# Kernel optimization log

Measured on AMD Instinct MI355X. Metric: run time of the kernel, lower is better.

## Reference

```python
import jax, jax.numpy as jnp
import numpy as np

N, E, B, BLOCK = 100000, 1600000, 8, 12500
IN, HID, K, OUT = 128, 128, 4, 2
EPS = 1e-15


def setup_inputs() -> dict:
    key = jax.random.key(0)
    ks = jax.random.split(key, 14)
    x = jax.random.normal(ks[0], (N, IN), jnp.float32)
    # edges constrained within each graph's contiguous node block
    src = jax.random.randint(ks[1], (E,), 0, N)
    off = jax.random.randint(ks[2], (E,), 0, BLOCK)
    dst = (src // BLOCK) * BLOCK + off
    edge_index = jnp.stack([src, dst])
    batch = jnp.arange(N) // BLOCK
    s = 0.02
    params = dict(
        W_root1=jax.random.normal(ks[3], (IN, HID), jnp.float32) * s,
        W_rel1=jax.random.normal(ks[4], (IN, HID), jnp.float32) * s,
        b_rel1=jnp.zeros((HID,), jnp.float32),
        W_pool=jax.random.normal(ks[5], (HID, K), jnp.float32) * s,
        b_pool=jnp.zeros((K,), jnp.float32),
        W_rel3=jax.random.normal(ks[6], (HID, HID), jnp.float32) * s,
        b_rel3=jnp.zeros((HID,), jnp.float32),
        W_root3=jax.random.normal(ks[7], (HID, HID), jnp.float32) * s,
        W_lin1=jax.random.normal(ks[8], (HID, HID), jnp.float32) * s,
        b_lin1=jnp.zeros((HID,), jnp.float32),
        W_lin2=jax.random.normal(ks[9], (HID, OUT), jnp.float32) * s,
        b_lin2=jnp.zeros((OUT,), jnp.float32),
    )
    return dict(x=x, edge_index=edge_index, batch=batch, **params)


def _forward(x, edge_index, batch, W_root1, W_rel1, b_rel1, W_pool, b_pool,
             W_rel3, b_rel3, W_root3, W_lin1, b_lin1, W_lin2, b_lin2):
    src, dst = edge_index[0], edge_index[1]
    # GraphConv (aggr='add'): lin_rel(sum_j x_j) + lin_root(x)
    agg = jax.ops.segment_sum(x[src], dst, num_segments=N)  # [N, IN]
    h = jax.nn.relu(agg @ W_rel1 + b_rel1 + x @ W_root1)    # [N, HID]
    # cluster assignment
    s = jax.nn.softmax(h @ W_pool + b_pool, axis=-1)        # [N, K]
    # pooled node features: out[b] = S_b^T X_b  -> [B, K, HID]
    out = jax.ops.segment_sum(s[:, :, None] * h[:, None, :], batch, num_segments=B)
    # coarsened adjacency: out_adj[b] = S_b^T A_b S_b (A[dst, src] = 1 per edge)
    e_graph = batch[dst]
    contrib = s[dst][:, :, None] * s[src][:, None, :]       # [E, K, K]
    out_adj = jax.ops.segment_sum(contrib, e_graph, num_segments=B)  # [B, K, K]
    # mincut loss
    mincut_num = jnp.einsum('bkk->b', out_adj)
    deg = jax.ops.segment_sum(jnp.ones((E,), x.dtype), dst, num_segments=N)
    mincut_den = jax.ops.segment_sum(deg * jnp.sum(s * s, axis=-1), batch, num_segments=B)
    mc_loss = jnp.mean(-(mincut_num / mincut_den))
    # orthogonality loss
    ss = jax.ops.segment_sum(s[:, :, None] * s[:, None, :], batch, num_segments=B)  # [B,K,K]
    ss_norm = jnp.linalg.norm(ss, axis=(1, 2), keepdims=True)
    i_s = jnp.eye(K, dtype=x.dtype)
    o_loss = jnp.mean(jnp.linalg.norm(ss / ss_norm - i_s / jnp.sqrt(jnp.float32(K)), axis=(1, 2)))
    # fix and normalize coarsened adjacency
    out_adj = out_adj * (1.0 - i_s)  # zero diagonal
    d = jnp.sqrt(jnp.sum(out_adj, axis=-1)) + EPS  # [B, K]
    out_adj = out_adj / d[:, None, :] / d[:, :, None]
    # DenseGraphConv (aggr='add'): lin_rel(adj @ x) + lin_root(x)
    x2 = jnp.einsum('bkl,blc->bkc', out_adj, out) @ W_rel3 + b_rel3 + out @ W_root3
    x2 = jnp.mean(x2, axis=1)  # [B, HID]
    x2 = jax.nn.relu(x2 @ W_lin1 + b_lin1)
    logits = x2 @ W_lin2 + b_lin2
    return jax.nn.log_softmax(logits, axis=-1), mc_loss, o_loss, s, out_adj


def reference(x, edge_index, batch, W_root1, W_rel1, b_rel1, W_pool, b_pool,
              W_rel3, b_rel3, W_root3, W_lin1, b_lin1, W_lin2, b_lin2):
    return _forward(x, edge_index, batch, W_root1, W_rel1, b_rel1, W_pool, b_pool,
                    W_rel3, b_rel3, W_root3, W_lin1, b_lin1, W_lin2, b_lin2)
```

## Files before the change

kernel.cpp:

```cpp
#include <hip/hip_runtime.h>

#define NN     100000
#define EE     1600000
#define NB     8
#define BLK    12500
#define HID    128
#define KC     4
#define CHUNKS 196
#define NTILE  49
#define NBIN   392
#define GCAPS  5120

typedef __attribute__((ext_vector_type(8))) short bf16x8;
typedef __attribute__((ext_vector_type(4))) float f32x4;

__device__ __forceinline__ ushort f2bf(float f) {
  uint u = __float_as_uint(f);
  return (ushort)((u + 0x7FFFu + ((u >> 16) & 1u)) >> 16);
}
__device__ __forceinline__ float bf2f(ushort h) {
  return __uint_as_float(((uint)h) << 16);
}

__global__ __launch_bounds__(256) void k_prep_x(const float4* __restrict__ x4,
                                                ushort* __restrict__ xb) {
  int i = blockIdx.x * 256 + threadIdx.x;
  float4 v = x4[i];
  ushort4 r;
  r.x = f2bf(v.x); r.y = f2bf(v.y); r.z = f2bf(v.z); r.w = f2bf(v.w);
  *(ushort4*)(xb + (size_t)i * 4) = r;
}

__global__ __launch_bounds__(256) void k_prep_w(const float* __restrict__ Wrel1,
                                                const float* __restrict__ Wroot1,
                                                ushort* __restrict__ Wt) {
  int col = blockIdx.x, k = threadIdx.x;
  float v = (k < 128) ? Wrel1[k * 128 + col] : Wroot1[(k - 128) * 128 + col];
  Wt[col * 256 + k] = f2bf(v);
}

__global__ __launch_bounds__(256) void k_bucket2(const int* __restrict__ ei,
                                                 int* __restrict__ sbcnt,
                                                 uint* __restrict__ gbuf) {
  __shared__ uint stage[8192];
  __shared__ int cnt[NBIN], start[NBIN + 1], rbase[NBIN];
  __shared__ int gtot[8], gb[8];
  const int t = threadIdx.x;
  for (int b = t; b < NBIN; b += 256) cnt[b] = 0;
  __syncthreads();
  const int e0 = blockIdx.x * 8192;
  uint pk[32]; int br[32];
#pragma unroll
  for (int i = 0; i < 32; ++i) {
    int e = e0 + i * 256 + t;
    bool val = (e < EE);
    int src = 0, dst = 0;
    if (val) {
      src = __builtin_nontemporal_load(ei + e);
      dst = __builtin_nontemporal_load(ei + EE + e);
    }
    int g = dst / BLK;
    int dl = dst - g * BLK;
    int sl = src - g * BLK;
    int bin = g * NTILE + (dl >> 8);
    pk[i] = ((uint)sl << 16) | (uint)dl;
    br[i] = val ? ((bin << 14) | atomicAdd(&cnt[bin], 1)) : -1;
  }
  __syncthreads();
  if (t < 8) {
    int s = 0;
    for (int k = 0; k < NTILE; ++k) s += cnt[t * NTILE + k];
    gtot[t] = s;
  }
  __syncthreads();
  if (t == 0) {
    int s = 0;
    for (int g = 0; g < 8; ++g) { gb[g] = s; s += gtot[g]; }
    start[NBIN] = s;
  }
  __syncthreads();
  if (t < 8) {
    int run = gb[t];
    for (int k = 0; k < NTILE; ++k) { start[t * NTILE + k] = run; run += cnt[t * NTILE + k]; }
  }
  __syncthreads();
  for (int b = t; b < NBIN; b += 256) rbase[b] = atomicAdd(&sbcnt[b], cnt[b]);
#pragma unroll
  for (int i = 0; i < 32; ++i) {
    if (br[i] >= 0) {
      int bin = br[i] >> 14, rank = br[i] & 16383;
      stage[start[bin] + rank] = pk[i];
    }
  }
  __syncthreads();
  const int total = start[NBIN];
  for (int j = t; j < total; j += 256) {
    int lo = 0, hi = NBIN - 1;
    while (lo < hi) { int mid = (lo + hi + 1) >> 1; if (j >= start[mid]) lo = mid; else hi = mid - 1; }
    gbuf[(size_t)lo * GCAPS + rbase[lo] + (j - start[lo])] = stage[j];
  }
}

__global__ __launch_bounds__(512) void k_scan392(const int* __restrict__ sbcnt,
                                                 int* __restrict__ sbbase) {
  __shared__ int sd[512];
  const int t = threadIdx.x;
  int v = (t < NBIN) ? sbcnt[t] : 0;
  sd[t] = v;
  __syncthreads();
  for (int s = 1; s < 512; s <<= 1) {
    int x = (t >= s) ? sd[t - s] : 0;
    __syncthreads();
    sd[t] += x;
    __syncthreads();
  }
  if (t < NBIN) sbbase[t] = sd[t] - v;
}

__global__ __launch_bounds__(256) void k_csr_tile(const uint* __restrict__ gbuf,
                                                  const int* __restrict__ sbcnt,
                                                  const int* __restrict__ sbbase,
                                                  int* __restrict__ rowptr,
                                                  int* __restrict__ count,
                                                  int* __restrict__ csr) {
  const int g = blockIdx.x & 7;
  const int tile = blockIdx.x >> 3;
  const int bin = g * NTILE + tile;
  const int m = sbcnt[bin];
  const int base = sbbase[bin];
  const int n0t = tile * 256;
  const int nt = min(256, BLK - n0t);
  __shared__ uint ent[GCAPS];
  __shared__ ushort srt[GCAPS];
  __shared__ int cnt[256], scn[256], cur[256];
  const int t = threadIdx.x;
  cnt[t] = 0;
  __syncthreads();
  const uint* buf = gbuf + (size_t)bin * GCAPS;
  for (int i = t; i < m; i += 256) {
    uint pk = buf[i];
    ent[i] = pk;
    atomicAdd(&cnt[(int)(pk & 0xFFFFu) - n0t], 1);
  }
  __syncthreads();
  int v = cnt[t];
  scn[t] = v;
  __syncthreads();
  for (int s = 1; s < 256; s <<= 1) {
    int x = (t >= s) ? scn[t - s] : 0;
    __syncthreads();
    scn[t] += x;
    __syncthreads();
  }
  int excl = scn[t] - v;
  cur[t] = excl;
  if (t < nt) {
    rowptr[g * BLK + n0t + t] = base + excl;
    count[g * BLK + n0t + t] = v;
  }
  __syncthreads();
  for (int i = t; i < m; i += 256) {
    uint pk = ent[i];
    int p = atomicAdd(&cur[(int)(pk & 0xFFFFu) - n0t], 1);
    srt[p] = (ushort)(pk >> 16);
  }
  __syncthreads();
  const int nb = g * BLK;
  for (int i = t; i < m; i += 256)
    csr[base + i] = nb + (int)srt[i];
}

__global__ __launch_bounds__(256) void k_agg2(const ushort* __restrict__ xb,
                                              const int* __restrict__ count,
                                              const int* __restrict__ rowptr,
                                              const int* __restrict__ csr,
                                              ushort* __restrict__ aggb) {
  const int xg = blockIdx.x & 7;
  const int j = blockIdx.x >> 3;
  const int half = threadIdx.x >> 5;
  const int lane = threadIdx.x & 31;
  const int ln = j * 8 + half;
  if (ln >= BLK) return;
  const int node = xg * BLK + ln;
  const int deg = count[node];
  const int* sl = csr + rowptr[node];
  int idx0 = (lane < deg) ? sl[lane] : 0;
  int idx1 = (32 + lane < deg) ? sl[32 + lane] : 0;

#define GETIDX(e) ((e) < 32 ? __shfl(idx0, (e), 32) \
                            : ((e) < 64 ? __shfl(idx1, (e) - 32, 32) : sl[(e)]))

  float A0 = 0.f, A1 = 0.f, A2 = 0.f, A3 = 0.f;
  float B0 = 0.f, B1 = 0.f, B2 = 0.f, B3 = 0.f;
  float C0 = 0.f, C1 = 0.f, C2 = 0.f, C3 = 0.f;
  float D0 = 0.f, D1 = 0.f, D2 = 0.f, D3 = 0.f;
  int e = 0;
  for (; e + 4 <= deg; e += 4) {
    int s0 = GETIDX(e + 0);
    int s1 = GETIDX(e + 1);
    int s2 = GETIDX(e + 2);
    int s3 = GETIDX(e + 3);
    ushort4 v0 = *(const ushort4*)(xb + (size_t)s0 * HID + lane * 4);
    ushort4 v1 = *(const ushort4*)(xb + (size_t)s1 * HID + lane * 4);
    ushort4 v2 = *(const ushort4*)(xb + (size_t)s2 * HID + lane * 4);
    ushort4 v3 = *(const ushort4*)(xb + (size_t)s3 * HID + lane * 4);
    A0 += bf2f(v0.x); A1 += bf2f(v0.y); A2 += bf2f(v0.z); A3 += bf2f(v0.w);
    B0 += bf2f(v1.x); B1 += bf2f(v1.y); B2 += bf2f(v1.z); B3 += bf2f(v1.w);
    C0 += bf2f(v2.x); C1 += bf2f(v2.y); C2 += bf2f(v2.z); C3 += bf2f(v2.w);
    D0 += bf2f(v3.x); D1 += bf2f(v3.y); D2 += bf2f(v3.z); D3 += bf2f(v3.w);
  }
  for (; e < deg; ++e) {
    int s0 = GETIDX(e);
    ushort4 v0 = *(const ushort4*)(xb + (size_t)s0 * HID + lane * 4);
    A0 += bf2f(v0.x); A1 += bf2f(v0.y); A2 += bf2f(v0.z); A3 += bf2f(v0.w);
  }
#undef GETIDX

  ushort* dstp = aggb + (size_t)node * HID + lane * 4;
  {
    volatile const uint* pr = (volatile const uint*)dstp;
    uint d0 = pr[0];
    uint d1 = pr[1];
    (void)d0; (void)d1;
  }
  ushort4 r;
  r.x = f2bf(A0 + B0 + C0 + D0);
  r.y = f2bf(A1 + B1 + C1 + D1);
  r.z = f2bf(A2 + B2 + C2 + D2);
  r.w = f2bf(A3 + B3 + C3 + D3);
  *(ushort4*)dstp = r;
}

__global__ __launch_bounds__(256) void k_fused(
    const ushort* __restrict__ aggb, const ushort* __restrict__ xb,
    const ushort* __restrict__ Wt, const float* __restrict__ brel1,
    const float* __restrict__ Wpool, const float* __restrict__ bpool,
    const int* __restrict__ count, float* __restrict__ s_out,
    float* __restrict__ out_pool, float* __restrict__ ss_g,
    float* __restrict__ den_g) {
  __shared__ float hL[64][132];
  __shared__ float outL[KC][HID];
  __shared__ float ssL[16];
  __shared__ float denL;

  const int t = threadIdx.x;
  const int bi = blockIdx.x;
  const int bG = bi & 7;
  const int chunk = bi >> 3;
  const int node0 = bG * BLK + chunk * 64;
  int nrows = BLK - chunk * 64;
  if (nrows > 64) nrows = 64;

  for (int i = t; i < KC * HID; i += 256) ((float*)outL)[i] = 0.f;
  if (t < 16) ssL[t] = 0.f;
  if (t == 0) denL = 0.f;

  const int w = t >> 6;
  const int l = t & 63;
  const int m16 = l & 15;
  const int gq = l >> 4;

  bf16x8 Breg[8][2];
#pragma unroll
  for (int kt = 0; kt < 8; ++kt)
#pragma unroll
    for (int fc = 0; fc < 2; ++fc)
      Breg[kt][fc] =
          *(const bf16x8*)(Wt + (size_t)(32 * w + 16 * fc + m16) * 256 + kt * 32 + 8 * gq);

  const ushort* Arow_ag[4];
  const ushort* Arow_x[4];
#pragma unroll
  for (int fr = 0; fr < 4; ++fr) {
    int r = 16 * fr + m16;
    if (r >= nrows) r = nrows - 1;
    Arow_ag[fr] = aggb + (size_t)(node0 + r) * HID + 8 * gq;
    Arow_x[fr]  = xb   + (size_t)(node0 + r) * HID + 8 * gq;
  }

  f32x4 acc[4][2];
#pragma unroll
  for (int fr = 0; fr < 4; ++fr)
#pragma unroll
    for (int fc = 0; fc < 2; ++fc) acc[fr][fc] = (f32x4){0.f, 0.f, 0.f, 0.f};

#pragma unroll
  for (int kt = 0; kt < 8; ++kt) {
    const int off = (kt & 3) * 32;
    bf16x8 af[4];
#pragma unroll
    for (int fr = 0; fr < 4; ++fr)
      af[fr] = *(const bf16x8*)((kt < 4 ? Arow_ag[fr] : Arow_x[fr]) + off);
#pragma unroll
    for (int fr = 0; fr < 4; ++fr)
#pragma unroll
      for (int fc = 0; fc < 2; ++fc)
        acc[fr][fc] = __builtin_amdgcn_mfma_f32_16x16x32_bf16(af[fr], Breg[kt][fc],
                                                              acc[fr][fc], 0, 0, 0);
  }

  const float bc0 = brel1[32 * w + m16];
  const float bc1 = brel1[32 * w + 16 + m16];
#pragma unroll
  for (int fr = 0; fr < 4; ++fr)
#pragma unroll
    for (int fc = 0; fc < 2; ++fc)
#pragma unroll
      for (int r = 0; r < 4; ++r)
        hL[16 * fr + 4 * gq + r][32 * w + 16 * fc + m16] =
            fmaxf(acc[fr][fc][r] + (fc ? bc1 : bc0), 0.f);
  __syncthreads();

  const int g4 = t >> 4;
  const int c0 = (t & 15) << 2;
  const int li = t & 15;

  float h[4][8];
#pragma unroll
  for (int r = 0; r < 4; ++r) {
    float4 v0 = *(const float4*)&hL[g4 * 4 + r][c0];
    float4 v1 = *(const float4*)&hL[g4 * 4 + r][c0 + 64];
    h[r][0] = v0.x; h[r][1] = v0.y; h[r][2] = v0.z; h[r][3] = v0.w;
    h[r][4] = v1.x; h[r][5] = v1.y; h[r][6] = v1.z; h[r][7] = v1.w;
  }

  float wp[8][4];
#pragma unroll
  for (int j = 0; j < 8; ++j) {
    int col = c0 + (j & 3) + (j >> 2) * 64;
    float4 v = *(const float4*)(Wpool + col * 4);
    wp[j][0] = v.x; wp[j][1] = v.y; wp[j][2] = v.z; wp[j][3] = v.w;
  }
  float pp[4][4];
#pragma unroll
  for (int r = 0; r < 4; ++r)
#pragma unroll
    for (int k = 0; k < 4; ++k) pp[r][k] = 0.f;
#pragma unroll
  for (int r = 0; r < 4; ++r)
#pragma unroll
    for (int j = 0; j < 8; ++j)
#pragma unroll
      for (int k = 0; k < 4; ++k) pp[r][k] = fmaf(h[r][j], wp[j][k], pp[r][k]);
#pragma unroll
  for (int m = 1; m <= 8; m <<= 1)
#pragma unroll
    for (int r = 0; r < 4; ++r)
#pragma unroll
      for (int k = 0; k < 4; ++k) pp[r][k] += __shfl_xor(pp[r][k], m);

  float4 bp4 = *(const float4*)bpool;
  float bp[4] = {bp4.x, bp4.y, bp4.z, bp4.w};
  float sv[4][4];
#pragma unroll
  for (int r = 0; r < 4; ++r) {
    float p[4];
#pragma unroll
    for (int k = 0; k < 4; ++k) p[k] = pp[r][k] + bp[k];
    float mx = fmaxf(fmaxf(p[0], p[1]), fmaxf(p[2], p[3]));
    float e0 = expf(p[0] - mx), e1 = expf(p[1] - mx), e2 = expf(p[2] - mx), e3 = expf(p[3] - mx);
    float inv = 1.f / (e0 + e1 + e2 + e3);
    float valid = (g4 * 4 + r < nrows) ? 1.f : 0.f;
    sv[r][0] = e0 * inv * valid; sv[r][1] = e1 * inv * valid;
    sv[r][2] = e2 * inv * valid; sv[r][3] = e3 * inv * valid;
  }

  {
    int rW = li >> 2, kW = li & 3;
    if (g4 * 4 + rW < nrows) {
      int node = node0 + g4 * 4 + rW;
      float val = 0.f;
#pragma unroll
      for (int rr = 0; rr < 4; ++rr)
#pragma unroll
        for (int kk = 0; kk < 4; ++kk)
          if (li == rr * 4 + kk) val = sv[rr][kk];
      s_out[node * 4 + kW] = val;
    }
  }

  {
    int k1 = li >> 2, k2 = li & 3;
    float a1[4], a2[4];
#pragma unroll
    for (int rr = 0; rr < 4; ++rr) {
      float v1 = 0.f, v2 = 0.f;
#pragma unroll
      for (int kk = 0; kk < 4; ++kk) {
        if (k1 == kk) v1 = sv[rr][kk];
        if (k2 == kk) v2 = sv[rr][kk];
      }
      a1[rr] = v1; a2[rr] = v2;
    }
    float ssv = a1[0] * a2[0] + a1[1] * a2[1] + a1[2] * a2[2] + a1[3] * a2[3];
    atomicAdd(&ssL[li], ssv);
  }

  if (li == 0) {
    float dent = 0.f;
#pragma unroll
    for (int rr = 0; rr < 4; ++rr) {
      int rowg = g4 * 4 + rr;
      if (rowg < nrows) {
        float dg = (float)count[node0 + rowg];
        dent += dg * (sv[rr][0] * sv[rr][0] + sv[rr][1] * sv[rr][1] +
                      sv[rr][2] * sv[rr][2] + sv[rr][3] * sv[rr][3]);
      }
    }
    atomicAdd(&denL, dent);
  }

  float po[4][8];
#pragma unroll
  for (int k = 0; k < 4; ++k)
#pragma unroll
    for (int c = 0; c < 8; ++c) po[k][c] = 0.f;
#pragma unroll
  for (int k = 0; k < 4; ++k)
#pragma unroll
    for (int rr = 0; rr < 4; ++rr)
#pragma unroll
      for (int c = 0; c < 8; ++c) po[k][c] = fmaf(sv[rr][k], h[rr][c], po[k][c]);
#pragma unroll
  for (int k = 0; k < 4; ++k)
#pragma unroll
    for (int c = 0; c < 8; ++c) {
      po[k][c] += __shfl_xor(po[k][c], 16);
      po[k][c] += __shfl_xor(po[k][c], 32);
    }
  if ((t & 63) < 16) {
#pragma unroll
    for (int k = 0; k < 4; ++k)
#pragma unroll
      for (int c = 0; c < 8; ++c)
        atomicAdd(&outL[k][c0 + (c & 3) + (c >> 2) * 64], po[k][c]);
  }

  __syncthreads();
  for (int i = t; i < KC * HID; i += 256)
    atomicAdd(&out_pool[bG * KC * HID + i], ((const float*)outL)[i]);
  if (t < 16) atomicAdd(&ss_g[bG * 16 + t], ssL[t]);
  if (t == 0) atomicAdd(&den_g[bG], denL);
}

__global__ __launch_bounds__(256) void k_adj2(const int* __restrict__ count,
                                              const int* __restrict__ rowptr,
                                              const int* __restrict__ csr,
                                              const float* __restrict__ s,
                                              float* __restrict__ adjraw) {
  __shared__ float accL[4][2][16];
  const int t = threadIdx.x;
  if (t < 128) ((float*)accL)[t] = 0.f;
  __syncthreads();
  const int node = blockIdx.x * 256 + t;
  const int g0 = (blockIdx.x * 256) / BLK;
  if (node < NN) {
    const int gi = node / BLK - g0;
    const int deg = count[node];
    const int* sl = csr + rowptr[node];
    float A0 = 0.f, A1 = 0.f, A2 = 0.f, A3 = 0.f;
    float B0 = 0.f, B1 = 0.f, B2 = 0.f, B3 = 0.f;
    float C0 = 0.f, C1 = 0.f, C2 = 0.f, C3 = 0.f;
    float D0 = 0.f, D1 = 0.f, D2 = 0.f, D3 = 0.f;
    int e = 0;
    for (; e + 4 <= deg; e += 4) {
      int s0 = sl[e + 0], s1 = sl[e + 1], s2 = sl[e + 2], s3 = sl[e + 3];
      float4 v0 = *(const float4*)(s + (size_t)s0 * 4);
      float4 v1 = *(const float4*)(s + (size_t)s1 * 4);
      float4 v2 = *(const float4*)(s + (size_t)s2 * 4);
      float4 v3 = *(const float4*)(s + (size_t)s3 * 4);
      A0 += v0.x; A1 += v0.y; A2 += v0.z; A3 += v0.w;
      B0 += v1.x; B1 += v1.y; B2 += v1.z; B3 += v1.w;
      C0 += v2.x; C1 += v2.y; C2 += v2.z; C3 += v2.w;
      D0 += v3.x; D1 += v3.y; D2 += v3.z; D3 += v3.w;
    }
    for (; e < deg; ++e) {
      float4 v0 = *(const float4*)(s + (size_t)sl[e] * 4);
      A0 += v0.x; A1 += v0.y; A2 += v0.z; A3 += v0.w;
    }
    float t0 = A0 + B0 + C0 + D0;
    float t1 = A1 + B1 + C1 + D1;
    float t2 = A2 + B2 + C2 + D2;
    float t3 = A3 + B3 + C3 + D3;
    float4 sn = *(const float4*)(s + (size_t)node * 4);
    float* base = accL[t >> 6][gi];
#pragma unroll
    for (int i = 0; i < 16; ++i) {
      int idx = (i + t) & 15;
      int hi = idx >> 2, lo = idx & 3;
      float a = (hi == 0) ? sn.x : (hi == 1) ? sn.y : (hi == 2) ? sn.z : sn.w;
      float b = (lo == 0) ? t0 : (lo == 1) ? t1 : (lo == 2) ? t2 : t3;
      atomicAdd(base + idx, a * b);
    }
  }
  __syncthreads();
  if (t < 32) {
    int gi = t >> 4, i = t & 15, gg = g0 + gi;
    if (gg < NB) {
      float v = accL[0][gi][i] + accL[1][gi][i] + accL[2][gi][i] + accL[3][gi][i];
      atomicAdd(&adjraw[gg * 16 + i], v);
    }
  }
}

__global__ __launch_bounds__(128) void k_graph(
    const float* __restrict__ out_pool, const float* __restrict__ adjraw,
    const float* __restrict__ den_g, const float* __restrict__ ss_g,
    const float* __restrict__ Wrel3, const float* __restrict__ brel3,
    const float* __restrict__ Wroot3, const float* __restrict__ Wlin1,
    const float* __restrict__ blin1, const float* __restrict__ Wlin2,
    const float* __restrict__ blin2, float* __restrict__ d_out,
    float* __restrict__ scratch) {
  const int b = blockIdx.x, t = threadIdx.x;
  __shared__ float adjL[16], adjnL[16], dL[4];
  __shared__ float osL[128], msL[128], x2mL[128], x3L[128];
  if (t < 16) adjL[t] = adjraw[b * 16 + t];
  __syncthreads();
  if (t < 4) {
    float srow = 0.f;
#pragma unroll
    for (int l = 0; l < 4; ++l)
      if (l != t) srow += adjL[t * 4 + l];
    dL[t] = sqrtf(srow) + 1e-15f;
  }
  __syncthreads();
  if (t < 16) {
    int k1 = t >> 2, k2 = t & 3;
    float az = (k1 == k2) ? 0.f : adjL[t];
    float an = az / (dL[k2] * dL[k1]);
    adjnL[t] = an;
    d_out[400018 + b * 16 + t] = an;
  }
  __syncthreads();
  float o0 = out_pool[b * 512 + 0 * 128 + t];
  float o1 = out_pool[b * 512 + 1 * 128 + t];
  float o2 = out_pool[b * 512 + 2 * 128 + t];
  float o3 = out_pool[b * 512 + 3 * 128 + t];
  float m0 = adjnL[0] * o0 + adjnL[1] * o1 + adjnL[2] * o2 + adjnL[3] * o3;
  float m1 = adjnL[4] * o0 + adjnL[5] * o1 + adjnL[6] * o2 + adjnL[7] * o3;
  float m2 = adjnL[8] * o0 + adjnL[9] * o1 + adjnL[10] * o2 + adjnL[11] * o3;
  float m3 = adjnL[12] * o0 + adjnL[13] * o1 + adjnL[14] * o2 + adjnL[15] * o3;
  osL[t] = o0 + o1 + o2 + o3;
  msL[t] = m0 + m1 + m2 + m3;
  __syncthreads();
  float accc = brel3[t];
  for (int j = 0; j < 128; ++j)
    accc += 0.25f * (msL[j] * Wrel3[j * 128 + t] + osL[j] * Wroot3[j * 128 + t]);
  x2mL[t] = accc;
  __syncthreads();
  float a2 = blin1[t];
  for (int j = 0; j < 128; ++j) a2 += x2mL[j] * Wlin1[j * 128 + t];
  x3L[t] = fmaxf(a2, 0.f);
  __syncthreads();
  if (t < 2) {
    float lg = blin2[t];
    for (int j = 0; j < 128; ++j) lg += x3L[j] * Wlin2[j * 2 + t];
    scratch[b * 2 + t] = lg;
  }
  if (t == 0) {
    float tr = adjL[0] + adjL[5] + adjL[10] + adjL[15];
    scratch[16 + b] = tr / den_g[b];
    float n2 = 0.f;
    for (int i = 0; i < 16; ++i) { float v = ss_g[b * 16 + i]; n2 += v * v; }
    float nn = sqrtf(n2);
    float od = 0.f;
    for (int i = 0; i < 16; ++i) {
      float v = ss_g[b * 16 + i] / nn - (((i >> 2) == (i & 3)) ? 0.5f : 0.f);
      od += v * v;
    }
    scratch[24 + b] = sqrtf(od);
  }
}

__global__ void k_final(const float* __restrict__ scratch, float* __restrict__ d_out) {
  if (threadIdx.x == 0 && blockIdx.x == 0) {
    float mc = 0.f, oo = 0.f;
    for (int b = 0; b < NB; ++b) { mc += scratch[16 + b]; oo += scratch[24 + b]; }
    d_out[16] = -(mc / (float)NB);
    d_out[17] = oo / (float)NB;
    for (int b = 0; b < NB; ++b) {
      float l0 = scratch[2 * b], l1 = scratch[2 * b + 1];
      float m = fmaxf(l0, l1);
      float lse = m + logf(expf(l0 - m) + expf(l1 - m));
      d_out[2 * b] = l0 - lse;
      d_out[2 * b + 1] = l1 - lse;
    }
  }
}

extern "C" void kernel_launch(void* const* d_in, const int* in_sizes, int n_in,
                              void* d_out, int out_size, void* d_ws, size_t ws_size,
                              hipStream_t stream) {
  (void)in_sizes; (void)n_in; (void)out_size; (void)ws_size;
  const float* x      = (const float*)d_in[0];
  const int*   ei     = (const int*)d_in[1];
  const float* Wroot1 = (const float*)d_in[3];
  const float* Wrel1  = (const float*)d_in[4];
  const float* brel1  = (const float*)d_in[5];
  const float* Wpool  = (const float*)d_in[6];
  const float* bpool  = (const float*)d_in[7];
  const float* Wrel3  = (const float*)d_in[8];
  const float* brel3  = (const float*)d_in[9];
  const float* Wroot3 = (const float*)d_in[10];
  const float* Wlin1  = (const float*)d_in[11];
  const float* blin1  = (const float*)d_in[12];
  const float* Wlin2  = (const float*)d_in[13];
  const float* blin2  = (const float*)d_in[14];
  float* out = (float*)d_out;

  char* ws = (char*)d_ws;
  float*  out_pool = (float*)(ws + 0);
  float*  ss_g     = (float*)(ws + 16384);
  float*  adjraw   = (float*)(ws + 16896);
  float*  den_g    = (float*)(ws + 17408);
  float*  scratch  = (float*)(ws + 17440);
  int*    sbcnt    = (int*)(ws + 17568);
  int*    sbbase   = (int*)(ws + 19136);
  int*    count    = (int*)(ws + 20736);
  int*    rowptr   = (int*)(ws + 420736);
  ushort* Wt       = (ushort*)(ws + 820752);
  int*    csr      = (int*)(ws + 886288);
  ushort* xb       = (ushort*)(ws + 7286288);
  ushort* aggb     = (ushort*)(ws + 32886288);
  uint*   gbuf     = (uint*)(ws + 58486288);

  hipMemsetAsync(ws, 0, 19136, stream);
  k_prep_x<<<12500, 256, 0, stream>>>((const float4*)x, xb);
  k_prep_w<<<128, 256, 0, stream>>>(Wrel1, Wroot1, Wt);
  k_bucket2<<<196, 256, 0, stream>>>(ei, sbcnt, gbuf);
  k_scan392<<<1, 512, 0, stream>>>(sbcnt, sbbase);
  k_csr_tile<<<NBIN, 256, 0, stream>>>(gbuf, sbcnt, sbbase, rowptr, count, csr);
  k_agg2<<<8 * ((BLK + 7) / 8), 256, 0, stream>>>(xb, count, rowptr, csr, aggb);
  k_fused<<<NB * CHUNKS, 256, 0, stream>>>(aggb, xb, Wt, brel1, Wpool, bpool, count,
                                           out + 18, out_pool, ss_g, den_g);
  k_adj2<<<(NN + 255) / 256, 256, 0, stream>>>(count, rowptr, csr, out + 18, adjraw);
  k_graph<<<NB, 128, 0, stream>>>(out_pool, adjraw, den_g, ss_g, Wrel3, brel3, Wroot3,
                                  Wlin1, blin1, Wlin2, blin2, out, scratch);
  k_final<<<1, 64, 0, stream>>>(scratch, out);
}
```

Measured before the change: 224.7 us.

## Stage GEMM A-tiles in LDS via global_load_lds with XOR swizzle, store h as bf16

The fused kernel now copies the 64-row aggregate and x tiles into shared memory with direct global-to-LDS loads, using an XOR swizzle to avoid bank conflicts. The MFMA loop then reads its A fragments from LDS instead of issuing strided global loads. The h tile is kept in shared memory as bf16 instead of fp32, which cuts LDS footprint but adds a rounding step before pooling. It also drops a dummy volatile read of the destination in the aggregation kernel.

Measured after the change: 212.7 us. -5.3%, faster.

```diff
diff --git a/kernel.cpp b/kernel.cpp
--- a/kernel.cpp
+++ b/kernel.cpp
@@ -21,6 +21,10 @@
 __device__ __forceinline__ float bf2f(ushort h) {
   return __uint_as_float(((uint)h) << 16);
 }
+
+#define GLL16(g, l) \
+  __builtin_amdgcn_global_load_lds((const __attribute__((address_space(1))) void*)(g), \
+                                   (__attribute__((address_space(3))) void*)(l), 16, 0, 0)
 
 __global__ __launch_bounds__(256) void k_prep_x(const float4* __restrict__ x4,
                                                 ushort* __restrict__ xb) {
@@ -217,12 +221,6 @@
 #undef GETIDX
 
   ushort* dstp = aggb + (size_t)node * HID + lane * 4;
-  {
-    volatile const uint* pr = (volatile const uint*)dstp;
-    uint d0 = pr[0];
-    uint d1 = pr[1];
-    (void)d0; (void)d1;
-  }
   ushort4 r;
   r.x = f2bf(A0 + B0 + C0 + D0);
   r.y = f2bf(A1 + B1 + C1 + D1);
@@ -238,7 +236,9 @@
     const int* __restrict__ count, float* __restrict__ s_out,
     float* __restrict__ out_pool, float* __restrict__ ss_g,
     float* __restrict__ den_g) {
-  __shared__ float hL[64][132];
+  __shared__ ushort Aag_s[64][128];
+  __shared__ ushort Ax_s[64][128];
+  __shared__ ushort hLb[64][136];
   __shared__ float outL[KC][HID];
   __shared__ float ssL[16];
   __shared__ float denL;
@@ -251,12 +251,29 @@
   int nrows = BLK - chunk * 64;
   if (nrows > 64) nrows = 64;
 
+  const int w = t >> 6;
+  const int l = t & 63;
+
+  {
+    const int sub = l >> 4;
+    const int c16 = l & 15;
+#pragma unroll
+    for (int i = 0; i < 4; ++i) {
+      const int j = w * 4 + i;
+      const int row = j * 4 + sub;
+      const int rs = (row < nrows) ? row : (nrows - 1);
+      const int boff = (c16 * 16) ^ ((row & 7) << 4);
+      const ushort* ga = aggb + (size_t)(node0 + rs) * HID + (boff >> 1);
+      const ushort* gx = xb + (size_t)(node0 + rs) * HID + (boff >> 1);
+      GLL16(ga, &Aag_s[j * 4][0]);
+      GLL16(gx, &Ax_s[j * 4][0]);
+    }
+  }
+
   for (int i = t; i < KC * HID; i += 256) ((float*)outL)[i] = 0.f;
   if (t < 16) ssL[t] = 0.f;
   if (t == 0) denL = 0.f;
 
-  const int w = t >> 6;
-  const int l = t & 63;
   const int m16 = l & 15;
   const int gq = l >> 4;
 
@@ -268,29 +285,26 @@
       Breg[kt][fc] =
           *(const bf16x8*)(Wt + (size_t)(32 * w + 16 * fc + m16) * 256 + kt * 32 + 8 * gq);
 
-  const ushort* Arow_ag[4];
-  const ushort* Arow_x[4];
-#pragma unroll
-  for (int fr = 0; fr < 4; ++fr) {
-    int r = 16 * fr + m16;
-    if (r >= nrows) r = nrows - 1;
-    Arow_ag[fr] = aggb + (size_t)(node0 + r) * HID + 8 * gq;
-    Arow_x[fr]  = xb   + (size_t)(node0 + r) * HID + 8 * gq;
-  }
-
   f32x4 acc[4][2];
 #pragma unroll
   for (int fr = 0; fr < 4; ++fr)
 #pragma unroll
     for (int fc = 0; fc < 2; ++fc) acc[fr][fc] = (f32x4){0.f, 0.f, 0.f, 0.f};
 
+  asm volatile("s_waitcnt vmcnt(0)" ::: "memory");
+  __syncthreads();
+
 #pragma unroll
   for (int kt = 0; kt < 8; ++kt) {
-    const int off = (kt & 3) * 32;
+    const int k4 = kt & 3;
     bf16x8 af[4];
 #pragma unroll
-    for (int fr = 0; fr < 4; ++fr)
-      af[fr] = *(const bf16x8*)((kt < 4 ? Arow_ag[fr] : Arow_x[fr]) + off);
+    for (int fr = 0; fr < 4; ++fr) {
+      const int r = 16 * fr + m16;
+      const int ci = (k4 * 32 + gq * 8) ^ ((r & 7) << 3);
+      af[fr] = (kt < 4) ? *(const bf16x8*)&Aag_s[r][ci]
+                        : *(const bf16x8*)&Ax_s[r][ci];
+    }
 #pragma unroll
     for (int fr = 0; fr < 4; ++fr)
 #pragma unroll
@@ -307,8 +321,8 @@
     for (int fc = 0; fc < 2; ++fc)
 #pragma unroll
       for (int r = 0; r < 4; ++r)
-        hL[16 * fr + 4 * gq + r][32 * w + 16 * fc + m16] =
-            fmaxf(acc[fr][fc][r] + (fc ? bc1 : bc0), 0.f);
+        hLb[16 * fr + 4 * gq + r][32 * w + 16 * fc + m16] =
+            f2bf(fmaxf(acc[fr][fc][r] + (fc ? bc1 : bc0), 0.f));
   __syncthreads();
 
   const int g4 = t >> 4;
@@ -318,10 +332,10 @@
   float h[4][8];
 #pragma unroll
   for (int r = 0; r < 4; ++r) {
-    float4 v0 = *(const float4*)&hL[g4 * 4 + r][c0];
-    float4 v1 = *(const float4*)&hL[g4 * 4 + r][c0 + 64];
-    h[r][0] = v0.x; h[r][1] = v0.y; h[r][2] = v0.z; h[r][3] = v0.w;
-    h[r][4] = v1.x; h[r][5] = v1.y; h[r][6] = v1.z; h[r][7] = v1.w;
+    ushort4 v0 = *(const ushort4*)&hLb[g4 * 4 + r][c0];
+    ushort4 v1 = *(const ushort4*)&hLb[g4 * 4 + r][c0 + 64];
+    h[r][0] = bf2f(v0.x); h[r][1] = bf2f(v0.y); h[r][2] = bf2f(v0.z); h[r][3] = bf2f(v0.w);
+    h[r][4] = bf2f(v1.x); h[r][5] = bf2f(v1.y); h[r][6] = bf2f(v1.z); h[r][7] = bf2f(v1.w);
   }
 
   float wp[8][4];
```
